# Optimization experiments

Measured on AMD Instinct MI355X. Metric: run time of the kernel, lower is better.

Reference implementation:

```python
import jax, jax.numpy as jnp
import numpy as np

N_NODES = 100000
N_EDGES = 3200000
F_IN, F_HID, N_CLASS = 512, 256, 41


def gcn_conv(x, edge_src, edge_dst, W, b, n_nodes):
    """PyG GCNConv: self-loops + symmetric deg^-1/2 normalization, then
    linear transform, gather-scale-scatter aggregation, bias add."""
    # add self loops
    loop = jnp.arange(n_nodes, dtype=edge_src.dtype)
    src = jnp.concatenate([edge_src, loop])
    dst = jnp.concatenate([edge_dst, loop])
    # degree (with self loops) on destination nodes
    deg = jax.ops.segment_sum(jnp.ones_like(dst, dtype=x.dtype), dst,
                              num_segments=n_nodes)
    dinv = deg ** -0.5  # deg >= 1 thanks to self loops
    norm = dinv[src] * dinv[dst]  # [E+N]
    h = x @ W  # [N, F_out]
    # gather-scale-scatter: out[dst] += norm * h[src]
    out = jax.ops.segment_sum(h[src] * norm[:, None], dst,
                              num_segments=n_nodes)
    return out + b


def setup_inputs() -> dict:
    key = jax.random.key(0)
    k1, k2, k3, k4 = jax.random.split(key, 4)
    x = jax.random.normal(k1, (N_NODES, F_IN), dtype=jnp.float32)
    edge_index = jax.random.randint(k2, (2, N_EDGES), 0, N_NODES, dtype=jnp.int64)
    W1 = jax.random.normal(k3, (F_IN, F_HID), dtype=jnp.float32) * (1.0 / np.sqrt(F_IN))
    b1 = jnp.zeros((F_HID,), dtype=jnp.float32)
    W2 = jax.random.normal(k4, (F_HID, N_CLASS), dtype=jnp.float32) * (1.0 / np.sqrt(F_HID))
    b2 = jnp.zeros((N_CLASS,), dtype=jnp.float32)
    return {"x": x, "edge_index": edge_index, "W1": W1, "b1": b1,
            "W2": W2, "b2": b2}


def reference(x, edge_index, W1, b1, W2, b2):
    src, dst = edge_index[0], edge_index[1]
    h = gcn_conv(x, src, dst, W1, b1, N_NODES)
    h = jax.nn.relu(h)
    # dropout omitted (eval mode / training=False)
    h = gcn_conv(h, src, dst, W2, b2, N_NODES)
    return jax.nn.log_softmax(h, axis=1)
```

## Files before the change

### kernel.cpp

```cpp
#include <hip/hip_runtime.h>
#include <math.h>

#define F_IN   512
#define F_HID  256
#define N_CLS  41

#define CHUNK  16384
#define MAXBK  3200
#define PKMASK 0x1FFFF
#define STILE_SH 12
#define NKEY   1024

typedef __attribute__((ext_vector_type(8))) short     bf16x8;
typedef __attribute__((ext_vector_type(8))) unsigned short u16x8;
typedef __attribute__((ext_vector_type(4))) float     f32x4;

__device__ __forceinline__ float b2f(unsigned short u) {
    union { unsigned int i; float f; } v; v.i = ((unsigned int)u) << 16; return v.f;
}
__device__ __forceinline__ unsigned short f2b(float f) {
    unsigned int u = __float_as_uint(f);
    u = (u + 0x7fffu + ((u >> 16) & 1u)) >> 16;
    return (unsigned short)u;
}

__global__ __launch_bounds__(256) void hist_pass(const int* __restrict__ edst,
                                                 int* __restrict__ hist_g,
                                                 int E, int NBK, int NW) {
    __shared__ int lh[MAXBK];
    int t = threadIdx.x, w = blockIdx.x;
    for (int b = t; b < NBK; b += 256) lh[b] = 0;
    __syncthreads();
    int e0 = w * CHUNK;
#pragma unroll 4
    for (int i = 0; i < CHUNK / 256; i++) {
        int e = e0 + i * 256 + t;
        if (e < E) atomicAdd(&lh[edst[e] >> 5], 1);
    }
    __syncthreads();
    for (int b = t; b < NBK; b += 256) hist_g[(size_t)b * NW + w] = lh[b];
}

__global__ __launch_bounds__(256) void s1_btot(const int* __restrict__ hist_g,
                                               int* __restrict__ btot,
                                               int NBK, int NW) {
    int b = blockIdx.x * 256 + threadIdx.x;
    if (b >= NBK) return;
    const int* row = &hist_g[(size_t)b * NW];
    int s = 0;
    for (int w = 0; w < NW; w++) s += row[w];
    btot[b] = s;
}

__global__ __launch_bounds__(256) void s2_scan(const int* __restrict__ btot,
                                               int* __restrict__ bbase, int NBK) {
    __shared__ int ls[MAXBK];
    __shared__ int ss[257];
    int t = threadIdx.x;
    const int CH = (MAXBK + 255) / 256;
    for (int b = t; b < NBK; b += 256) ls[b] = btot[b];
    __syncthreads();
    int s = 0;
    for (int i = 0; i < CH; i++) {
        int idx = t * CH + i;
        if (idx < NBK) s += ls[idx];
    }
    ss[t] = s;
    __syncthreads();
    if (t == 0) {
        int run = 0;
        for (int i = 0; i < 256; i++) { int v = ss[i]; ss[i] = run; run += v; }
        ss[256] = run;
    }
    __syncthreads();
    int run = ss[t];
    for (int i = 0; i < CH; i++) {
        int idx = t * CH + i;
        if (idx < NBK) { int v = ls[idx]; ls[idx] = run; run += v; }
    }
    __syncthreads();
    for (int b = t; b < NBK; b += 256) bbase[b] = ls[b];
    if (t == 0) bbase[NBK] = ss[256];
}

__global__ __launch_bounds__(256) void s3_rowscan(int* __restrict__ hist_g,
                                                  const int* __restrict__ bbase,
                                                  int NBK, int NW) {
    int b = blockIdx.x * 256 + threadIdx.x;
    if (b >= NBK) return;
    int* row = &hist_g[(size_t)b * NW];
    int run = bbase[b];
    for (int w = 0; w < NW; w++) { int v = row[w]; row[w] = run; run += v; }
}

__global__ __launch_bounds__(256) void scatter_pass(const int* __restrict__ esrc,
                                                    const int* __restrict__ edst,
                                                    const int* __restrict__ hist_g,
                                                    int* __restrict__ packed,
                                                    int E, int NBK, int NW) {
    __shared__ int cur[MAXBK];
    int t = threadIdx.x, w = blockIdx.x;
    for (int b = t; b < NBK; b += 256) cur[b] = hist_g[(size_t)b * NW + w];
    __syncthreads();
    int e0 = w * CHUNK;
#pragma unroll 4
    for (int i = 0; i < CHUNK / 256; i++) {
        int e = e0 + i * 256 + t;
        if (e < E) {
            int d = edst[e];
            int pos = atomicAdd(&cur[d >> 5], 1);
            packed[pos] = esrc[e] | ((d & 31) << 17);
        }
    }
}

__global__ __launch_bounds__(256) void bucket_sort(const int* __restrict__ packed,
                                                   const int* __restrict__ bbase,
                                                   int* __restrict__ packed2,
                                                   int* __restrict__ rp,
                                                   float* __restrict__ dinv, int M) {
    __shared__ int cnt[NKEY];
    __shared__ int ss[256];
    __shared__ int rtot[32];
    int b = blockIdx.x, t = threadIdx.x;
    int start = bbase[b], end = bbase[b + 1];
    for (int i = t; i < NKEY; i += 256) cnt[i] = 0;
    __syncthreads();
    for (int e = start + t; e < end; e += 256) {
        int p = packed[e];
        atomicAdd(&cnt[(((p >> 17) & 31) << 5) | ((p & PKMASK) >> STILE_SH)], 1);
    }
    __syncthreads();
    if (t < 32) {
        int s = 0;
#pragma unroll
        for (int i = 0; i < 32; i++) s += cnt[(t << 5) + i];
        rtot[t] = s;
        int node = (b << 5) + t;
        if (node < M) dinv[node] = rsqrtf((float)s + 1.0f);
    }
    int i0 = t << 2;
    int v0 = cnt[i0], v1 = cnt[i0 + 1], v2 = cnt[i0 + 2], v3 = cnt[i0 + 3];
    ss[t] = v0 + v1 + v2 + v3;
    __syncthreads();
    if (t == 0) {
        int run = start;
#pragma unroll
        for (int i = 0; i < 32; i++) {
            run += rtot[i];
            int node = (b << 5) + i;
            if (node < M) rp[node] = run;
        }
        run = start;
        for (int i = 0; i < 256; i++) { int v = ss[i]; ss[i] = run; run += v; }
    }
    __syncthreads();
    int run = ss[t];
    cnt[i0] = run; run += v0;
    cnt[i0 + 1] = run; run += v1;
    cnt[i0 + 2] = run; run += v2;
    cnt[i0 + 3] = run;
    __syncthreads();
    for (int e = start + t; e < end; e += 256) {
        int p = packed[e];
        int pos = atomicAdd(&cnt[(((p >> 17) & 31) << 5) | ((p & PKMASK) >> STILE_SH)], 1);
        packed2[pos] = p;
    }
}


__global__ __launch_bounds__(256) void cvt_W1t(const float* __restrict__ W1,
                                               unsigned short* __restrict__ W1t) {
    int n = blockIdx.x;
    for (int k = threadIdx.x; k < F_IN; k += 256)
        W1t[n * F_IN + k] = f2b(W1[(size_t)k * F_HID + n]);
}

__global__ __launch_bounds__(256) void cvt_W2t(const float* __restrict__ W2,
                                               unsigned short* __restrict__ W2t) {
    int n = blockIdx.x;
    int k = threadIdx.x;
    W2t[n * F_HID + k] = (n < N_CLS) ? f2b(W2[(size_t)k * N_CLS + n])
                                     : (unsigned short)0;
}


__global__ __launch_bounds__(512) void mfma_gemm1(const float* __restrict__ A,
                                                  const unsigned short* __restrict__ Bt,
                                                  const float* __restrict__ dinv,
                                                  unsigned short* __restrict__ H1,
                                                  int M) {
    __shared__ unsigned short As[128 * 40];
    __shared__ unsigned short Bs[256 * 40];
    int tid = threadIdx.x;
    int wave = tid >> 6, lane = tid & 63;
    int quad = lane >> 4, l15 = lane & 15;
    int m0 = blockIdx.x * 128;
    int wm = (wave & 1) * 64, wn = (wave >> 1) * 64;

    f32x4 acc[4][4] = {};

    int ar = tid >> 2, aq = tid & 3;
    int bn = tid >> 1, bc = tid & 1;

    for (int k0 = 0; k0 < F_IN; k0 += 32) {
        {
            int gm = m0 + ar;
            float4 v0, v1;
            if (gm < M) {
                const float4* ap = (const float4*)&A[(size_t)gm * F_IN + k0 + aq * 8];
                v0 = ap[0]; v1 = ap[1];
            } else {
                v0 = v1 = make_float4(0.f, 0.f, 0.f, 0.f);
            }
            u16x8 w;
            w[0]=f2b(v0.x); w[1]=f2b(v0.y); w[2]=f2b(v0.z); w[3]=f2b(v0.w);
            w[4]=f2b(v1.x); w[5]=f2b(v1.y); w[6]=f2b(v1.z); w[7]=f2b(v1.w);
            *(u16x8*)&As[ar * 40 + aq * 8] = w;
        }
        {
            const unsigned short* bp = &Bt[(size_t)bn * F_IN + k0];
            *(u16x8*)&Bs[bn * 40 + bc * 8]       = *(const u16x8*)(bp + bc * 8);
            *(u16x8*)&Bs[bn * 40 + (bc + 2) * 8] = *(const u16x8*)(bp + bc * 8 + 16);
        }
        __syncthreads();
        bf16x8 af[4], bfr[4];
#pragma unroll
        for (int i = 0; i < 4; i++)
            af[i] = *(const bf16x8*)&As[(wm + i * 16 + l15) * 40 + quad * 8];
#pragma unroll
        for (int j = 0; j < 4; j++)
            bfr[j] = *(const bf16x8*)&Bs[(wn + j * 16 + l15) * 40 + quad * 8];
#pragma unroll
        for (int i = 0; i < 4; i++)
#pragma unroll
            for (int j = 0; j < 4; j++)
                acc[i][j] = __builtin_amdgcn_mfma_f32_16x16x32_bf16(
                    af[i], bfr[j], acc[i][j], 0, 0, 0);
        __syncthreads();
    }
#pragma unroll
    for (int i = 0; i < 4; i++) {
#pragma unroll
        for (int rr = 0; rr < 4; rr++) {
            int gm = m0 + wm + i * 16 + quad * 4 + rr;
            if (gm < M) {
                float dv = dinv[gm];
#pragma unroll
                for (int j = 0; j < 4; j++) {
                    int gn = wn + j * 16 + l15;
                    H1[(size_t)gm * F_HID + gn] = f2b(dv * acc[i][j][rr]);
                }
            }
        }
    }
}


__global__ __launch_bounds__(256) void csr_agg1(const int* __restrict__ rp,
                                                const int* __restrict__ col,
                                                const float* __restrict__ dinv,
                                                const unsigned short* __restrict__ h1,
                                                const float* __restrict__ b1,
                                                unsigned short* __restrict__ act1,
                                                int M) {
    int w = threadIdx.x >> 6, lane = threadIdx.x & 63;
    int r = blockIdx.x * 4 + w;
    if (r >= M) return;
    int start = r ? rp[r - 1] : 0;
    int end = rp[r];
    float dr = dinv[r];

    const ushort4* hv = (const ushort4*)h1;
    ushort4 v = hv[(size_t)r * 64 + lane];
    float ax = b2f(v.x), ay = b2f(v.y), az = b2f(v.z), aw = b2f(v.w);

    int e = start;
    for (; e + 8 <= end; e += 8) {
        int s0 = col[e]     & PKMASK, s1 = col[e + 1] & PKMASK;
        int s2 = col[e + 2] & PKMASK, s3 = col[e + 3] & PKMASK;
        int s4 = col[e + 4] & PKMASK, s5 = col[e + 5] & PKMASK;
        int s6 = col[e + 6] & PKMASK, s7 = col[e + 7] & PKMASK;
        ushort4 q0 = hv[(size_t)s0 * 64 + lane];
        ushort4 q1 = hv[(size_t)s1 * 64 + lane];
        ushort4 q2 = hv[(size_t)s2 * 64 + lane];
        ushort4 q3 = hv[(size_t)s3 * 64 + lane];
        ushort4 q4 = hv[(size_t)s4 * 64 + lane];
        ushort4 q5 = hv[(size_t)s5 * 64 + lane];
        ushort4 q6 = hv[(size_t)s6 * 64 + lane];
        ushort4 q7 = hv[(size_t)s7 * 64 + lane];
        ax += ((b2f(q0.x) + b2f(q1.x)) + (b2f(q2.x) + b2f(q3.x)))
            + ((b2f(q4.x) + b2f(q5.x)) + (b2f(q6.x) + b2f(q7.x)));
        ay += ((b2f(q0.y) + b2f(q1.y)) + (b2f(q2.y) + b2f(q3.y)))
            + ((b2f(q4.y) + b2f(q5.y)) + (b2f(q6.y) + b2f(q7.y)));
        az += ((b2f(q0.z) + b2f(q1.z)) + (b2f(q2.z) + b2f(q3.z)))
            + ((b2f(q4.z) + b2f(q5.z)) + (b2f(q6.z) + b2f(q7.z)));
        aw += ((b2f(q0.w) + b2f(q1.w)) + (b2f(q2.w) + b2f(q3.w)))
            + ((b2f(q4.w) + b2f(q5.w)) + (b2f(q6.w) + b2f(q7.w)));
    }
    for (; e < end; e++) {
        ushort4 q = hv[(size_t)(col[e] & PKMASK) * 64 + lane];
        ax += b2f(q.x); ay += b2f(q.y); az += b2f(q.z); aw += b2f(q.w);
    }
    float4 bb = *(const float4*)&b1[lane * 4];
    ushort4 o;
    o.x = f2b(fmaxf(dr * ax + bb.x, 0.f));
    o.y = f2b(fmaxf(dr * ay + bb.y, 0.f));
    o.z = f2b(fmaxf(dr * az + bb.z, 0.f));
    o.w = f2b(fmaxf(dr * aw + bb.w, 0.f));
    ((ushort4*)act1)[(size_t)r * 64 + lane] = o;
}


__global__ __launch_bounds__(256) void mfma_gemm2(const unsigned short* __restrict__ act1,
                                                  const unsigned short* __restrict__ W2t,
                                                  const float* __restrict__ dinv,
                                                  float* __restrict__ h2, int M) {
    int wave = threadIdx.x >> 6, lane = threadIdx.x & 63;
    int quad = lane >> 4, l15 = lane & 15;
    int r0 = (blockIdx.x * 4 + wave) * 16;
    if (r0 >= M) return;

    f32x4 acc[3] = {};
    const unsigned short* arow = &act1[(size_t)(r0 + l15) * F_HID];
#pragma unroll
    for (int kt = 0; kt < F_HID; kt += 32) {
        bf16x8 af = *(const bf16x8*)&arow[kt + quad * 8];
#pragma unroll
        for (int j = 0; j < 3; j++) {
            bf16x8 bf = *(const bf16x8*)&W2t[(size_t)(j * 16 + l15) * F_HID + kt + quad * 8];
            acc[j] = __builtin_amdgcn_mfma_f32_16x16x32_bf16(af, bf, acc[j], 0, 0, 0);
        }
    }
#pragma unroll
    for (int j = 0; j < 3; j++) {
        int c = j * 16 + l15;
        if (c < N_CLS) {
#pragma unroll
            for (int rr = 0; rr < 4; rr++) {
                int r = r0 + quad * 4 + rr;
                h2[(size_t)r * N_CLS + c] = dinv[r] * acc[j][rr];
            }
        }
    }
}


__global__ __launch_bounds__(256) void csr_agg2_lsm(const int* __restrict__ rp,
                                                    const int* __restrict__ col,
                                                    const float* __restrict__ dinv,
                                                    const float* __restrict__ h2,
                                                    const float* __restrict__ b2,
                                                    float* __restrict__ out, int M) {
    int w = threadIdx.x >> 6, lane = threadIdx.x & 63;
    int r = blockIdx.x * 4 + w;
    if (r >= M) return;
    int start = r ? rp[r - 1] : 0;
    int end = rp[r];
    float dr = dinv[r];

    float acc = 0.f;
    if (lane < N_CLS) acc = h2[(size_t)r * N_CLS + lane];
    int e = start;
    for (; e + 4 <= end; e += 4) {
        int s0 = col[e] & PKMASK,     s1 = col[e + 1] & PKMASK;
        int s2 = col[e + 2] & PKMASK, s3 = col[e + 3] & PKMASK;
        if (lane < N_CLS) {
            float a0 = h2[(size_t)s0 * N_CLS + lane];
            float a1 = h2[(size_t)s1 * N_CLS + lane];
            float a2 = h2[(size_t)s2 * N_CLS + lane];
            float a3 = h2[(size_t)s3 * N_CLS + lane];
            acc += (a0 + a1) + (a2 + a3);
        }
    }
    for (; e < end; e++) {
        if (lane < N_CLS) acc += h2[(size_t)(col[e] & PKMASK) * N_CLS + lane];
    }
    float v = (lane < N_CLS) ? dr * acc + b2[lane] : -INFINITY;

    float m = v;
#pragma unroll
    for (int off = 32; off; off >>= 1) m = fmaxf(m, __shfl_xor(m, off));
    float ex = (lane < N_CLS) ? expf(v - m) : 0.f;
    float s = ex;
#pragma unroll
    for (int off = 32; off; off >>= 1) s += __shfl_xor(s, off);
    float ls = logf(s);
    if (lane < N_CLS) out[(size_t)r * N_CLS + lane] = v - m - ls;
}


extern "C" void kernel_launch(void* const* d_in, const int* in_sizes, int n_in,
                              void* d_out, int out_size, void* d_ws, size_t ws_size,
                              hipStream_t stream) {
    const float* x  = (const float*)d_in[0];
    const int*   ei = (const int*)d_in[1];
    const float* W1 = (const float*)d_in[2];
    const float* b1 = (const float*)d_in[3];
    const float* W2 = (const float*)d_in[4];
    const float* b2 = (const float*)d_in[5];
    float* out = (float*)d_out;

    const int M = in_sizes[0] / F_IN;
    const int E = in_sizes[1] / 2;
    const int* esrc = ei;
    const int* edst = ei + E;

    const int NBK = (M + 31) / 32;
    const int NW  = (E + CHUNK - 1) / CHUNK;

    char* ws = (char*)d_ws;
    float*          dinv    = (float*)(ws);
    int*            rp      = (int*)  (ws +    400128);
    int*            bbase   = (int*)  (ws +    800256);
    int*            btot    = (int*)  (ws +    812800);
    int*            hist_g  = (int*)  (ws +    825344);
    int*            packed  = (int*)  (ws +   3275392ull);
    int*            packed2 = (int*)  (ws +  16075392ull);
    unsigned short* W1t     = (unsigned short*)(ws + 28875392ull);
    unsigned short* W2t     = (unsigned short*)(ws + 29137536ull);
    unsigned short* h1      = (unsigned short*)(ws + 29162112ull);
    unsigned short* act1    = (unsigned short*)(ws + 80362112ull);
    float*          h2      = (float*)(ws + 131562112ull);

    hist_pass<<<NW, 256, 0, stream>>>(edst, hist_g, E, NBK, NW);
    s1_btot<<<(NBK + 255) / 256, 256, 0, stream>>>(hist_g, btot, NBK, NW);
    s2_scan<<<1, 256, 0, stream>>>(btot, bbase, NBK);
    s3_rowscan<<<(NBK + 255) / 256, 256, 0, stream>>>(hist_g, bbase, NBK, NW);
    scatter_pass<<<NW, 256, 0, stream>>>(esrc, edst, hist_g, packed, E, NBK, NW);
    bucket_sort<<<NBK, 256, 0, stream>>>(packed, bbase, packed2, rp, dinv, M);

    cvt_W1t<<<F_HID, 256, 0, stream>>>(W1, W1t);
    cvt_W2t<<<48, 256, 0, stream>>>(W2, W2t);

    mfma_gemm1<<<(M + 127) / 128, 512, 0, stream>>>(x, W1t, dinv, h1, M);
    csr_agg1<<<(M + 3) / 4, 256, 0, stream>>>(rp, packed2, dinv, h1, b1, act1, M);

    mfma_gemm2<<<(M / 16 + 3) / 4, 256, 0, stream>>>(act1, W2t, dinv, h2, M);
    csr_agg2_lsm<<<(M + 3) / 4, 256, 0, stream>>>(rp, packed2, dinv, h2, b2, out, M);
}
```

Before: 955.4 us.

## Split H1 into 64-column feature slabs and aggregate each slab in a separate pass

The first GEMM now writes H1 in a feature-slab layout of four 64-column slabs, each a contiguous [M,64] array. The first aggregation kernel is launched with four times as many blocks, each handling one slab with one bf16 per lane. The aim is cache locality: each pass gathers from a 12.8MB slab that can stay resident in L2/LLC instead of the full 51MB table. In exchange, the CSR indices are re-read four times, each gather is a narrower 128-byte row segment, and GEMM1's stores become more scattered.

New measurement: 1.084 ms. +13.5%, slower.

```diff
diff --git a/kernel.cpp b/kernel.cpp
--- a/kernel.cpp
+++ b/kernel.cpp
@@ -249,7 +249,8 @@
 #pragma unroll
                 for (int j = 0; j < 4; j++) {
                     int gn = wn + j * 16 + l15;
-                    H1[(size_t)gm * F_HID + gn] = f2b(dv * acc[i][j][rr]);
+                    H1[((size_t)(gn >> 6) * M + gm) * 64 + (gn & 63)] =
+                        f2b(dv * acc[i][j][rr]);
                 }
             }
         }
@@ -265,15 +266,16 @@
                                                 unsigned short* __restrict__ act1,
                                                 int M) {
     int w = threadIdx.x >> 6, lane = threadIdx.x & 63;
-    int r = blockIdx.x * 4 + w;
+    int nrb = (M + 3) >> 2;
+    int pass = blockIdx.x / nrb;
+    int r = (blockIdx.x - pass * nrb) * 4 + w;
     if (r >= M) return;
     int start = r ? rp[r - 1] : 0;
     int end = rp[r];
     float dr = dinv[r];
 
-    const ushort4* hv = (const ushort4*)h1;
-    ushort4 v = hv[(size_t)r * 64 + lane];
-    float ax = b2f(v.x), ay = b2f(v.y), az = b2f(v.z), aw = b2f(v.w);
+    const unsigned short* hb = h1 + (size_t)pass * M * 64;
+    float a = b2f(hb[(size_t)r * 64 + lane]);
 
     int e = start;
     for (; e + 8 <= end; e += 8) {
@@ -281,34 +283,21 @@
         int s2 = col[e + 2] & PKMASK, s3 = col[e + 3] & PKMASK;
         int s4 = col[e + 4] & PKMASK, s5 = col[e + 5] & PKMASK;
         int s6 = col[e + 6] & PKMASK, s7 = col[e + 7] & PKMASK;
-        ushort4 q0 = hv[(size_t)s0 * 64 + lane];
-        ushort4 q1 = hv[(size_t)s1 * 64 + lane];
-        ushort4 q2 = hv[(size_t)s2 * 64 + lane];
-        ushort4 q3 = hv[(size_t)s3 * 64 + lane];
-        ushort4 q4 = hv[(size_t)s4 * 64 + lane];
-        ushort4 q5 = hv[(size_t)s5 * 64 + lane];
-        ushort4 q6 = hv[(size_t)s6 * 64 + lane];
-        ushort4 q7 = hv[(size_t)s7 * 64 + lane];
-        ax += ((b2f(q0.x) + b2f(q1.x)) + (b2f(q2.x) + b2f(q3.x)))
-            + ((b2f(q4.x) + b2f(q5.x)) + (b2f(q6.x) + b2f(q7.x)));
-        ay += ((b2f(q0.y) + b2f(q1.y)) + (b2f(q2.y) + b2f(q3.y)))
-            + ((b2f(q4.y) + b2f(q5.y)) + (b2f(q6.y) + b2f(q7.y)));
-        az += ((b2f(q0.z) + b2f(q1.z)) + (b2f(q2.z) + b2f(q3.z)))
-            + ((b2f(q4.z) + b2f(q5.z)) + (b2f(q6.z) + b2f(q7.z)));
-        aw += ((b2f(q0.w) + b2f(q1.w)) + (b2f(q2.w) + b2f(q3.w)))
-            + ((b2f(q4.w) + b2f(q5.w)) + (b2f(q6.w) + b2f(q7.w)));
-    }
-    for (; e < end; e++) {
-        ushort4 q = hv[(size_t)(col[e] & PKMASK) * 64 + lane];
-        ax += b2f(q.x); ay += b2f(q.y); az += b2f(q.z); aw += b2f(q.w);
-    }
-    float4 bb = *(const float4*)&b1[lane * 4];
-    ushort4 o;
-    o.x = f2b(fmaxf(dr * ax + bb.x, 0.f));
-    o.y = f2b(fmaxf(dr * ay + bb.y, 0.f));
-    o.z = f2b(fmaxf(dr * az + bb.z, 0.f));
-    o.w = f2b(fmaxf(dr * aw + bb.w, 0.f));
-    ((ushort4*)act1)[(size_t)r * 64 + lane] = o;
+        float q0 = b2f(hb[(size_t)s0 * 64 + lane]);
+        float q1 = b2f(hb[(size_t)s1 * 64 + lane]);
+        float q2 = b2f(hb[(size_t)s2 * 64 + lane]);
+        float q3 = b2f(hb[(size_t)s3 * 64 + lane]);
+        float q4 = b2f(hb[(size_t)s4 * 64 + lane]);
+        float q5 = b2f(hb[(size_t)s5 * 64 + lane]);
+        float q6 = b2f(hb[(size_t)s6 * 64 + lane]);
+        float q7 = b2f(hb[(size_t)s7 * 64 + lane]);
+        a += ((q0 + q1) + (q2 + q3)) + ((q4 + q5) + (q6 + q7));
+    }
+    for (; e < end; e++)
+        a += b2f(hb[(size_t)(col[e] & PKMASK) * 64 + lane]);
+
+    float bv = b1[pass * 64 + lane];
+    act1[(size_t)r * F_HID + pass * 64 + lane] = f2b(fmaxf(dr * a + bv, 0.f));
 }
 
 
@@ -434,7 +423,10 @@
     cvt_W2t<<<48, 256, 0, stream>>>(W2, W2t);
 
     mfma_gemm1<<<(M + 127) / 128, 512, 0, stream>>>(x, W1t, dinv, h1, M);
-    csr_agg1<<<(M + 3) / 4, 256, 0, stream>>>(rp, packed2, dinv, h1, b1, act1, M);
+    {
+        const int nrb = (M + 3) / 4;
+        csr_agg1<<<4 * nrb, 256, 0, stream>>>(rp, packed2, dinv, h1, b1, act1, M);
+    }
 
     mfma_gemm2<<<(M / 16 + 3) / 4, 256, 0, stream>>>(act1, W2t, dinv, h2, M);
     csr_agg2_lsm<<<(M + 3) / 4, 256, 0, stream>>>(rp, packed2, dinv, h2, b2, out, M);
```

## Fuse layer-1 aggregation with layer-2 GEMM and gather bf16 padded h2

Applied to the files above, without the earlier changes.

The first-layer CSR aggregation now keeps each block's four activated rows in shared memory, and one wave runs the MFMA layer-2 projection on them. The result is written as bf16 into a 64-wide padded buffer, so neither the act1 intermediate nor a separate GEMM launch is needed. The second aggregation gathers 8-byte bf16 vectors, with four edge groups in parallel per wave, then reduces across the groups with shuffles and does a vectorized log-softmax with nontemporal stores. The cost is a block-wide sync, an MFMA on a 16-row tile where only 4 rows are useful, and reduced precision for h2.

New measurement: 889.3 us. 6.9% less time.

```diff
diff --git a/kernel.cpp b/kernel.cpp
--- a/kernel.cpp
+++ b/kernel.cpp
@@ -257,23 +257,32 @@
 }
 
 
-__global__ __launch_bounds__(256) void csr_agg1(const int* __restrict__ rp,
-                                                const int* __restrict__ col,
-                                                const float* __restrict__ dinv,
-                                                const unsigned short* __restrict__ h1,
-                                                const float* __restrict__ b1,
-                                                unsigned short* __restrict__ act1,
-                                                int M) {
+__global__ __launch_bounds__(256) void csr_agg1_fused(const int* __restrict__ rp,
+                                                      const int* __restrict__ col,
+                                                      const float* __restrict__ dinv,
+                                                      const unsigned short* __restrict__ h1,
+                                                      const float* __restrict__ b1,
+                                                      const unsigned short* __restrict__ W2t,
+                                                      unsigned short* __restrict__ h2b,
+                                                      int M) {
+    __shared__ unsigned short a4[4][256];
     int w = threadIdx.x >> 6, lane = threadIdx.x & 63;
     int r = blockIdx.x * 4 + w;
-    if (r >= M) return;
-    int start = r ? rp[r - 1] : 0;
-    int end = rp[r];
-    float dr = dinv[r];
+    bool valid = r < M;
+    int start = 0, end = 0;
+    float dr = 0.f;
+    if (valid) {
+        start = r ? rp[r - 1] : 0;
+        end = rp[r];
+        dr = dinv[r];
+    }
 
     const ushort4* hv = (const ushort4*)h1;
-    ushort4 v = hv[(size_t)r * 64 + lane];
-    float ax = b2f(v.x), ay = b2f(v.y), az = b2f(v.z), aw = b2f(v.w);
+    float ax = 0.f, ay = 0.f, az = 0.f, aw = 0.f;
+    if (valid) {
+        ushort4 v = hv[(size_t)r * 64 + lane];
+        ax = b2f(v.x); ay = b2f(v.y); az = b2f(v.z); aw = b2f(v.w);
+    }
 
     int e = start;
     for (; e + 8 <= end; e += 8) {
@@ -302,44 +311,41 @@
         ushort4 q = hv[(size_t)(col[e] & PKMASK) * 64 + lane];
         ax += b2f(q.x); ay += b2f(q.y); az += b2f(q.z); aw += b2f(q.w);
     }
-    float4 bb = *(const float4*)&b1[lane * 4];
-    ushort4 o;
-    o.x = f2b(fmaxf(dr * ax + bb.x, 0.f));
-    o.y = f2b(fmaxf(dr * ay + bb.y, 0.f));
-    o.z = f2b(fmaxf(dr * az + bb.z, 0.f));
-    o.w = f2b(fmaxf(dr * aw + bb.w, 0.f));
-    ((ushort4*)act1)[(size_t)r * 64 + lane] = o;
-}
-
-
-__global__ __launch_bounds__(256) void mfma_gemm2(const unsigned short* __restrict__ act1,
-                                                  const unsigned short* __restrict__ W2t,
-                                                  const float* __restrict__ dinv,
-                                                  float* __restrict__ h2, int M) {
-    int wave = threadIdx.x >> 6, lane = threadIdx.x & 63;
-    int quad = lane >> 4, l15 = lane & 15;
-    int r0 = (blockIdx.x * 4 + wave) * 16;
-    if (r0 >= M) return;
-
-    f32x4 acc[3] = {};
-    const unsigned short* arow = &act1[(size_t)(r0 + l15) * F_HID];
-#pragma unroll
-    for (int kt = 0; kt < F_HID; kt += 32) {
-        bf16x8 af = *(const bf16x8*)&arow[kt + quad * 8];
-#pragma unroll
-        for (int j = 0; j < 3; j++) {
-            bf16x8 bf = *(const bf16x8*)&W2t[(size_t)(j * 16 + l15) * F_HID + kt + quad * 8];
-            acc[j] = __builtin_amdgcn_mfma_f32_16x16x32_bf16(af, bf, acc[j], 0, 0, 0);
-        }
-    }
-#pragma unroll
-    for (int j = 0; j < 3; j++) {
-        int c = j * 16 + l15;
-        if (c < N_CLS) {
+    if (valid) {
+        float4 bb = *(const float4*)&b1[lane * 4];
+        ushort4 o;
+        o.x = f2b(fmaxf(dr * ax + bb.x, 0.f));
+        o.y = f2b(fmaxf(dr * ay + bb.y, 0.f));
+        o.z = f2b(fmaxf(dr * az + bb.z, 0.f));
+        o.w = f2b(fmaxf(dr * aw + bb.w, 0.f));
+        *(ushort4*)&a4[w][lane * 4] = o;
+    }
+    __syncthreads();
+    if (w == 0) {
+        int quad = lane >> 4, l15 = lane & 15;
+        int rr4 = l15 & 3;
+        f32x4 acc[3] = {};
+#pragma unroll
+        for (int kt = 0; kt < F_HID; kt += 32) {
+            bf16x8 af = *(const bf16x8*)&a4[rr4][kt + quad * 8];
+#pragma unroll
+            for (int j = 0; j < 3; j++) {
+                bf16x8 bf = *(const bf16x8*)&W2t[(size_t)(j * 16 + l15) * F_HID + kt + quad * 8];
+                acc[j] = __builtin_amdgcn_mfma_f32_16x16x32_bf16(af, bf, acc[j], 0, 0, 0);
+            }
+        }
+        if (quad == 0) {
 #pragma unroll
             for (int rr = 0; rr < 4; rr++) {
-                int r = r0 + quad * 4 + rr;
-                h2[(size_t)r * N_CLS + c] = dinv[r] * acc[j][rr];
+                int gr = blockIdx.x * 4 + rr;
+                if (gr < M) {
+                    float dv = dinv[gr];
+#pragma unroll
+                    for (int j = 0; j < 3; j++) {
+                        int c = j * 16 + l15;
+                        h2b[(size_t)gr * 64 + c] = f2b(dv * acc[j][rr]);
+                    }
+                }
             }
         }
     }
@@ -349,7 +355,7 @@
 __global__ __launch_bounds__(256) void csr_agg2_lsm(const int* __restrict__ rp,
                                                     const int* __restrict__ col,
                                                     const float* __restrict__ dinv,
-                                                    const float* __restrict__ h2,
+                                                    const unsigned short* __restrict__ h2b,
                                                     const float* __restrict__ b2,
                                                     float* __restrict__ out, int M) {
     int w = threadIdx.x >> 6, lane = threadIdx.x & 63;
@@ -358,35 +364,66 @@
     int start = r ? rp[r - 1] : 0;
     int end = rp[r];
     float dr = dinv[r];
-
-    float acc = 0.f;
-    if (lane < N_CLS) acc = h2[(size_t)r * N_CLS + lane];
+    int g = lane >> 4, l15 = lane & 15;
+    bool act = l15 < 11;
+
+    const ushort4* hq = (const ushort4*)h2b;
+    float a0 = 0.f, a1 = 0.f, a2 = 0.f, a3 = 0.f;
+    if (g == 0 && act) {
+        ushort4 q = hq[(size_t)r * 16 + l15];
+        a0 = b2f(q.x); a1 = b2f(q.y); a2 = b2f(q.z); a3 = b2f(q.w);
+    }
     int e = start;
-    for (; e + 4 <= end; e += 4) {
-        int s0 = col[e] & PKMASK,     s1 = col[e + 1] & PKMASK;
-        int s2 = col[e + 2] & PKMASK, s3 = col[e + 3] & PKMASK;
-        if (lane < N_CLS) {
-            float a0 = h2[(size_t)s0 * N_CLS + lane];
-            float a1 = h2[(size_t)s1 * N_CLS + lane];
-            float a2 = h2[(size_t)s2 * N_CLS + lane];
-            float a3 = h2[(size_t)s3 * N_CLS + lane];
-            acc += (a0 + a1) + (a2 + a3);
-        }
-    }
-    for (; e < end; e++) {
-        if (lane < N_CLS) acc += h2[(size_t)(col[e] & PKMASK) * N_CLS + lane];
-    }
-    float v = (lane < N_CLS) ? dr * acc + b2[lane] : -INFINITY;
-
-    float m = v;
-#pragma unroll
-    for (int off = 32; off; off >>= 1) m = fmaxf(m, __shfl_xor(m, off));
-    float ex = (lane < N_CLS) ? expf(v - m) : 0.f;
-    float s = ex;
-#pragma unroll
-    for (int off = 32; off; off >>= 1) s += __shfl_xor(s, off);
-    float ls = logf(s);
-    if (lane < N_CLS) out[(size_t)r * N_CLS + lane] = v - m - ls;
+    for (; e + 8 <= end; e += 8) {
+        int sA = col[e + g] & PKMASK;
+        int sB = col[e + 4 + g] & PKMASK;
+        if (act) {
+            ushort4 qA = hq[(size_t)sA * 16 + l15];
+            ushort4 qB = hq[(size_t)sB * 16 + l15];
+            a0 += b2f(qA.x) + b2f(qB.x);
+            a1 += b2f(qA.y) + b2f(qB.y);
+            a2 += b2f(qA.z) + b2f(qB.z);
+            a3 += b2f(qA.w) + b2f(qB.w);
+        }
+    }
+    if (e + g < end && act) {
+        ushort4 q = hq[(size_t)(col[e + g] & PKMASK) * 16 + l15];
+        a0 += b2f(q.x); a1 += b2f(q.y); a2 += b2f(q.z); a3 += b2f(q.w);
+    }
+    if (e + 4 + g < end && act) {
+        ushort4 q = hq[(size_t)(col[e + 4 + g] & PKMASK) * 16 + l15];
+        a0 += b2f(q.x); a1 += b2f(q.y); a2 += b2f(q.z); a3 += b2f(q.w);
+    }
+    a0 += __shfl_xor(a0, 16); a0 += __shfl_xor(a0, 32);
+    a1 += __shfl_xor(a1, 16); a1 += __shfl_xor(a1, 32);
+    a2 += __shfl_xor(a2, 16); a2 += __shfl_xor(a2, 32);
+    a3 += __shfl_xor(a3, 16); a3 += __shfl_xor(a3, 32);
+
+    int c0 = l15 * 4;
+    int cc = c0 < N_CLS ? c0 : N_CLS - 1;
+    float4 bb = make_float4(b2[cc], b2[(c0 + 1 < N_CLS) ? c0 + 1 : N_CLS - 1],
+                            b2[(c0 + 2 < N_CLS) ? c0 + 2 : N_CLS - 1],
+                            b2[(c0 + 3 < N_CLS) ? c0 + 3 : N_CLS - 1]);
+    float v0 = (c0     < N_CLS) ? dr * a0 + bb.x : -INFINITY;
+    float v1 = (c0 + 1 < N_CLS) ? dr * a1 + bb.y : -INFINITY;
+    float v2 = (c0 + 2 < N_CLS) ? dr * a2 + bb.z : -INFINITY;
+    float v3 = (c0 + 3 < N_CLS) ? dr * a3 + bb.w : -INFINITY;
+
+    float m = fmaxf(fmaxf(v0, v1), fmaxf(v2, v3));
+#pragma unroll
+    for (int off = 1; off < 16; off <<= 1) m = fmaxf(m, __shfl_xor(m, off));
+    float s = expf(v0 - m) + expf(v1 - m) + expf(v2 - m) + expf(v3 - m);
+#pragma unroll
+    for (int off = 1; off < 16; off <<= 1) s += __shfl_xor(s, off);
+    float ls = m + logf(s);
+
+    if (g == 0) {
+        float* orow = &out[(size_t)r * N_CLS];
+        if (c0 < N_CLS)     __builtin_nontemporal_store(v0 - ls, &orow[c0]);
+        if (c0 + 1 < N_CLS) __builtin_nontemporal_store(v1 - ls, &orow[c0 + 1]);
+        if (c0 + 2 < N_CLS) __builtin_nontemporal_store(v2 - ls, &orow[c0 + 2]);
+        if (c0 + 3 < N_CLS) __builtin_nontemporal_store(v3 - ls, &orow[c0 + 3]);
+    }
 }
 
 
@@ -420,8 +457,7 @@
     unsigned short* W1t     = (unsigned short*)(ws + 28875392ull);
     unsigned short* W2t     = (unsigned short*)(ws + 29137536ull);
     unsigned short* h1      = (unsigned short*)(ws + 29162112ull);
-    unsigned short* act1    = (unsigned short*)(ws + 80362112ull);
-    float*          h2      = (float*)(ws + 131562112ull);
+    unsigned short* h2b     = (unsigned short*)(ws + 80362112ull);
 
     hist_pass<<<NW, 256, 0, stream>>>(edst, hist_g, E, NBK, NW);
     s1_btot<<<(NBK + 255) / 256, 256, 0, stream>>>(hist_g, btot, NBK, NW);
@@ -434,8 +470,8 @@
     cvt_W2t<<<48, 256, 0, stream>>>(W2, W2t);
 
     mfma_gemm1<<<(M + 127) / 128, 512, 0, stream>>>(x, W1t, dinv, h1, M);
-    csr_agg1<<<(M + 3) / 4, 256, 0, stream>>>(rp, packed2, dinv, h1, b1, act1, M);
-
-    mfma_gemm2<<<(M / 16 + 3) / 4, 256, 0, stream>>>(act1, W2t, dinv, h2, M);
-    csr_agg2_lsm<<<(M + 3) / 4, 256, 0, stream>>>(rp, packed2, dinv, h2, b2, out, M);
-}
+    csr_agg1_fused<<<(M + 3) / 4, 256, 0, stream>>>(rp, packed2, dinv, h1, b1,
+                                                    W2t, h2b, M);
+
+    csr_agg2_lsm<<<(M + 3) / 4, 256, 0, stream>>>(rp, packed2, dinv, h2b, b2, out, M);
+}
```
